# Kernel optimization log

Hardware: AMD Instinct MI355X
Metric: run time of the kernel (lower is better)

The kernel has to match this reference:

```python
import jax, jax.numpy as jnp
import numpy as np

N_NODES = 50000
N_EDGES = 800000
D = 128


def setup_inputs() -> dict:
    key = jax.random.key(0)
    ks = jax.random.split(key, 8)
    scale = 1.0 / np.sqrt(D)
    return {
        "x": jax.random.normal(ks[0], (N_NODES, D), jnp.float32),
        "src": jax.random.randint(ks[1], (N_EDGES,), 0, N_NODES, jnp.int64 if jax.config.jax_enable_x64 else jnp.int32),
        "dst": jax.random.randint(ks[2], (N_EDGES,), 0, N_NODES, jnp.int64 if jax.config.jax_enable_x64 else jnp.int32),
        "W_self0": jax.random.normal(ks[3], (D, D), jnp.float32) * scale,
        "W_neigh0": jax.random.normal(ks[4], (D, D), jnp.float32) * scale,
        "b0": jnp.zeros((D,), jnp.float32),
        "W_self1": jax.random.normal(ks[5], (D, D), jnp.float32) * scale,
        "W_neigh1": jax.random.normal(ks[6], (D, D), jnp.float32) * scale,
        "b1": jnp.zeros((D,), jnp.float32),
    }


def _sage_conv(h, src, dst, W_self, W_neigh, b, n_nodes):
    # mean aggregation over incoming edges (DGL copy_u + mean; isolated nodes -> 0)
    msg = h[src]                                             # [E, d]
    agg = jax.ops.segment_sum(msg, dst, num_segments=n_nodes)  # [N, d]
    deg = jax.ops.segment_sum(jnp.ones((src.shape[0],), h.dtype), dst, num_segments=n_nodes)
    h_neigh = agg / jnp.maximum(deg, 1.0)[:, None]
    return h @ W_self + h_neigh @ W_neigh + b


def reference(x, src, dst, W_self0, W_neigh0, b0, W_self1, W_neigh1, b1):
    n = x.shape[0]
    h = jax.nn.relu(_sage_conv(x, src, dst, W_self0, W_neigh0, b0, n))
    h = jax.nn.relu(_sage_conv(h, src, dst, W_self1, W_neigh1, b1, n))
    # torch F.normalize(p=2, dim=1): x / max(||x||_2, eps)
    norm = jnp.sqrt(jnp.sum(h * h, axis=1, keepdims=True))
    return h / jnp.maximum(norm, 1e-12)
```

## Files before the change

### kernel.cpp

```cpp
#include <hip/hip_runtime.h>

#define NN 50000
#define D 128
#define BM 32
#define SL 6250

typedef unsigned int uint;
typedef unsigned short ushort;
typedef __attribute__((ext_vector_type(8))) short bf16x8;
typedef __attribute__((ext_vector_type(4))) float f32x4;

static __device__ __forceinline__ ushort f2bf(float f) {
    uint u = __float_as_uint(f);
    u = (u + 0x7FFFu + ((u >> 16) & 1u)) >> 16;
    return (ushort)u;
}

#define ADD8(a, u)                                                  \
    {                                                               \
        a[0] += __uint_as_float((u).x << 16);                       \
        a[1] += __uint_as_float((u).x & 0xFFFF0000u);               \
        a[2] += __uint_as_float((u).y << 16);                       \
        a[3] += __uint_as_float((u).y & 0xFFFF0000u);               \
        a[4] += __uint_as_float((u).z << 16);                       \
        a[5] += __uint_as_float((u).z & 0xFFFF0000u);               \
        a[6] += __uint_as_float((u).w << 16);                       \
        a[7] += __uint_as_float((u).w & 0xFFFF0000u);               \
    }

static __device__ __forceinline__ int ladr(int r, int ch) {
    return r * D + (((ch) ^ (r & 7)) << 3);
}

__global__ __launch_bounds__(256) void k_prep(
    const float* __restrict__ x, ushort* __restrict__ xb,
    const float* __restrict__ W0, const float* __restrict__ W1,
    const float* __restrict__ W2, const float* __restrict__ W3,
    ushort* __restrict__ P,
    const int* __restrict__ dst, int* __restrict__ hist, int E)
{
    const int bid = blockIdx.x;
    if (bid < 3125) {
        const int t = bid * 256 + threadIdx.x;
        const float4* p = reinterpret_cast<const float4*>(x) + (size_t)t * 2;
        const float4 v0 = p[0], v1 = p[1];
        uint4 u;
        u.x = (uint)f2bf(v0.x) | ((uint)f2bf(v0.y) << 16);
        u.y = (uint)f2bf(v0.z) | ((uint)f2bf(v0.w) << 16);
        u.z = (uint)f2bf(v1.x) | ((uint)f2bf(v1.y) << 16);
        u.w = (uint)f2bf(v1.z) | ((uint)f2bf(v1.w) << 16);
        reinterpret_cast<uint4*>(xb)[t] = u;
    } else if (bid < 3125 + 256) {
        const int o = (bid - 3125) * 256 + threadIdx.x;
        const int mat = o >> 14;
        const int idx = o & 16383;
        const int kt = idx >> 12;
        const int n  = (idx >> 5) & 127;
        const int ks = idx & 31;
        const float* W = (mat == 0) ? W0 : (mat == 1) ? W1 : (mat == 2) ? W2 : W3;
        P[o] = f2bf(W[(kt * 32 + ks) * D + n]);
    } else {
        const int hb = bid - (3125 + 256);
        const int s = hb & 7;
        const int lo = s * SL, hi = lo + SL;
        const int bs = hb >> 3;
        for (int e = bs * 256 + (int)threadIdx.x; e < E; e += 128 * 256) {
            const int d = dst[e];
            if (d >= lo && d < hi) atomicAdd(&hist[d], 1);
        }
    }
}

__global__ __launch_bounds__(256) void k_bsum(const int* __restrict__ hist,
                                              int* __restrict__ bsum, int n) {
    const int t = threadIdx.x;
    const int i0 = blockIdx.x * 512 + t * 2;
    int s = 0;
    if (i0 < n) s += hist[i0];
    if (i0 + 1 < n) s += hist[i0 + 1];
    #pragma unroll
    for (int o = 1; o < 64; o <<= 1) s += __shfl_xor(s, o);
    __shared__ int wsum[4];
    if ((t & 63) == 0) wsum[t >> 6] = s;
    __syncthreads();
    if (t == 0) bsum[blockIdx.x] = wsum[0] + wsum[1] + wsum[2] + wsum[3];
}

__global__ __launch_bounds__(128) void k_bscan(int* __restrict__ bsum, int nb) {
    const int t = threadIdx.x;
    const int lane = t & 63, w = t >> 6;
    int v = (t < nb) ? bsum[t] : 0;
    int inc = v;
    #pragma unroll
    for (int o = 1; o < 64; o <<= 1) { int u = __shfl_up(inc, o); if (lane >= o) inc += u; }
    __shared__ int wsum[2];
    if (lane == 63) wsum[w] = inc;
    __syncthreads();
    int off = (w == 1) ? wsum[0] : 0;
    if (t < nb) bsum[t] = off + inc - v;
}

__global__ __launch_bounds__(256) void k_apply(const int* __restrict__ hist,
        const int* __restrict__ bsum, int* __restrict__ row_off,
        int* __restrict__ cursor, int n, int E) {
    const int t = threadIdx.x;
    const int i0 = blockIdx.x * 512 + t * 2;
    const int v0 = (i0 < n) ? hist[i0] : 0;
    const int v1 = (i0 + 1 < n) ? hist[i0 + 1] : 0;
    const int s = v0 + v1;
    const int lane = t & 63, w = t >> 6;
    int inc = s;
    #pragma unroll
    for (int o = 1; o < 64; o <<= 1) { int u = __shfl_up(inc, o); if (lane >= o) inc += u; }
    __shared__ int wsum[4], woff[4];
    if (lane == 63) wsum[w] = inc;
    __syncthreads();
    if (t == 0) { int r = 0; for (int k = 0; k < 4; ++k) { woff[k] = r; r += wsum[k]; } }
    __syncthreads();
    const int ex = bsum[blockIdx.x] + woff[w] + (inc - s);
    if (i0 < n)     { row_off[i0] = ex;          cursor[i0] = ex; }
    if (i0 + 1 < n) { row_off[i0 + 1] = ex + v0; cursor[i0 + 1] = ex + v0; }
    if (blockIdx.x == 0 && t == 0) row_off[n] = E;
}

__global__ __launch_bounds__(256) void k_fill_s(const int* __restrict__ src,
        const int* __restrict__ dst, int* __restrict__ cursor,
        int* __restrict__ csr, int E) {
    const int s = blockIdx.x & 7;
    const int lo = s * SL, hi = lo + SL;
    const int bs = blockIdx.x >> 3;
    const int stride = (gridDim.x >> 3) * 256;
    for (int e = bs * 256 + (int)threadIdx.x; e < E; e += stride) {
        const int d = dst[e];
        const int sv = src[e];
        if (d >= lo && d < hi) {
            const int p = atomicAdd(&cursor[d], 1);
            csr[p] = sv;
        }
    }
}

template<bool NORM>
__global__ __launch_bounds__(512, 4) void k_sage(
    const ushort* __restrict__ hb,
    const int* __restrict__ csr, const int* __restrict__ row_off,
    const ushort* __restrict__ Wps, const ushort* __restrict__ Wpn,
    const float* __restrict__ bias, ushort* __restrict__ outb,
    float* __restrict__ out, int n, int E)
{
    __shared__ __align__(16) ushort hsb[BM * D];
    __shared__ __align__(16) ushort hnb[BM * D];
    __shared__ float outt[BM * 132];
    const int row0 = blockIdx.x * BM;
    const int tid = threadIdx.x;
    const int l = tid & 63;
    const int w = tid >> 6;

    {
        const int r = tid >> 4;
        const int ch = tid & 15;
        const int g = row0 + r;
        uint4 u = make_uint4(0u, 0u, 0u, 0u);
        if (g < n) u = *reinterpret_cast<const uint4*>(hb + (size_t)g * D + ch * 8);
        *reinterpret_cast<uint4*>(&hsb[ladr(r, ch)]) = u;
    }

    {
        const int r = tid >> 4;
        const int ql = tid & 15;
        const int g = row0 + r;
        int i = 0, e = 0;
        if (g < n) { i = row_off[g]; e = row_off[g + 1]; }
        const float invd = (e > i) ? 1.0f / (float)(e - i) : 0.0f;
        float a[8];
        #pragma unroll
        for (int j = 0; j < 8; ++j) a[j] = 0.f;
        const size_t off = (size_t)(ql * 8);
        for (; i + 3 < e; i += 4) {
            const int s0 = csr[i], s1 = csr[i + 1], s2 = csr[i + 2], s3 = csr[i + 3];
            const uint4 u0 = *reinterpret_cast<const uint4*>(hb + (size_t)s0 * D + off);
            const uint4 u1 = *reinterpret_cast<const uint4*>(hb + (size_t)s1 * D + off);
            const uint4 u2 = *reinterpret_cast<const uint4*>(hb + (size_t)s2 * D + off);
            const uint4 u3 = *reinterpret_cast<const uint4*>(hb + (size_t)s3 * D + off);
            ADD8(a, u0); ADD8(a, u1); ADD8(a, u2); ADD8(a, u3);
        }
        for (; i < e; ++i) {
            const int s0 = csr[i];
            const uint4 u0 = *reinterpret_cast<const uint4*>(hb + (size_t)s0 * D + off);
            ADD8(a, u0);
        }
        uint4 u;
        u.x = (uint)f2bf(a[0] * invd) | ((uint)f2bf(a[1] * invd) << 16);
        u.y = (uint)f2bf(a[2] * invd) | ((uint)f2bf(a[3] * invd) << 16);
        u.z = (uint)f2bf(a[4] * invd) | ((uint)f2bf(a[5] * invd) << 16);
        u.w = (uint)f2bf(a[6] * invd) | ((uint)f2bf(a[7] * invd) << 16);
        *reinterpret_cast<uint4*>(&hnb[ladr(r, ql)]) = u;
    }
    __syncthreads();

    {
        const int mt = w >> 2;
        const int ntA = (w & 3) * 2;
        const int rA = mt * 16 + (l & 15);
        const int kg = l >> 4;
        f32x4 acc0 = {0.f, 0.f, 0.f, 0.f};
        f32x4 acc1 = {0.f, 0.f, 0.f, 0.f};
        #pragma unroll
        for (int kt = 0; kt < 4; ++kt) {
            const int kc = kt * 4 + kg;
            const bf16x8 as = *reinterpret_cast<const bf16x8*>(&hsb[ladr(rA, kc)]);
            const bf16x8 an = *reinterpret_cast<const bf16x8*>(&hnb[ladr(rA, kc)]);
            const size_t wo0 = (size_t)(kt * 128 + ntA * 16 + (l & 15)) * 32 + kg * 8;
            const size_t wo1 = wo0 + 16 * 32;
            const bf16x8 bs0 = *reinterpret_cast<const bf16x8*>(Wps + wo0);
            const bf16x8 bn0 = *reinterpret_cast<const bf16x8*>(Wpn + wo0);
            const bf16x8 bs1 = *reinterpret_cast<const bf16x8*>(Wps + wo1);
            const bf16x8 bn1 = *reinterpret_cast<const bf16x8*>(Wpn + wo1);
            acc0 = __builtin_amdgcn_mfma_f32_16x16x32_bf16(as, bs0, acc0, 0, 0, 0);
            acc0 = __builtin_amdgcn_mfma_f32_16x16x32_bf16(an, bn0, acc0, 0, 0, 0);
            acc1 = __builtin_amdgcn_mfma_f32_16x16x32_bf16(as, bs1, acc1, 0, 0, 0);
            acc1 = __builtin_amdgcn_mfma_f32_16x16x32_bf16(an, bn1, acc1, 0, 0, 0);
        }
        const int c0 = ntA * 16 + (l & 15);
        const float bv0 = bias[c0], bv1 = bias[c0 + 16];
        #pragma unroll
        for (int i2 = 0; i2 < 4; ++i2) {
            const int rr = mt * 16 + kg * 4 + i2;
            outt[rr * 132 + c0]      = fmaxf(acc0[i2] + bv0, 0.f);
            outt[rr * 132 + c0 + 16] = fmaxf(acc1[i2] + bv1, 0.f);
        }
    }
    __syncthreads();

    {
        const int r = tid >> 4;
        const int c = (tid & 15) * 8;
        const int g = row0 + r;
        float4 v0 = *reinterpret_cast<const float4*>(&outt[r * 132 + c]);
        float4 v1 = *reinterpret_cast<const float4*>(&outt[r * 132 + c + 4]);
        if (!NORM) {
            if (g < n) {
                uint4 u;
                u.x = (uint)f2bf(v0.x) | ((uint)f2bf(v0.y) << 16);
                u.y = (uint)f2bf(v0.z) | ((uint)f2bf(v0.w) << 16);
                u.z = (uint)f2bf(v1.x) | ((uint)f2bf(v1.y) << 16);
                u.w = (uint)f2bf(v1.z) | ((uint)f2bf(v1.w) << 16);
                *reinterpret_cast<uint4*>(outb + (size_t)g * D + c) = u;
            }
        } else {
            float ssq = v0.x * v0.x + v0.y * v0.y + v0.z * v0.z + v0.w * v0.w
                      + v1.x * v1.x + v1.y * v1.y + v1.z * v1.z + v1.w * v1.w;
            #pragma unroll
            for (int o = 1; o < 16; o <<= 1) ssq += __shfl_xor(ssq, o);
            const float scale = 1.0f / fmaxf(sqrtf(ssq), 1e-12f);
            if (g < n) {
                v0.x *= scale; v0.y *= scale; v0.z *= scale; v0.w *= scale;
                v1.x *= scale; v1.y *= scale; v1.z *= scale; v1.w *= scale;
                *reinterpret_cast<float4*>(out + (size_t)g * D + c)     = v0;
                *reinterpret_cast<float4*>(out + (size_t)g * D + c + 4) = v1;
            }
        }
    }
}

extern "C" void kernel_launch(void* const* d_in, const int* in_sizes, int n_in,
                              void* d_out, int out_size, void* d_ws, size_t ws_size,
                              hipStream_t stream) {
    const float* x   = (const float*)d_in[0];
    const int*   src = (const int*)d_in[1];
    const int*   dst = (const int*)d_in[2];
    const float* Ws0 = (const float*)d_in[3];
    const float* Wn0 = (const float*)d_in[4];
    const float* b0  = (const float*)d_in[5];
    const float* Ws1 = (const float*)d_in[6];
    const float* Wn1 = (const float*)d_in[7];
    const float* b1  = (const float*)d_in[8];
    float* out = (float*)d_out;
    const int E = in_sizes[1];

    ushort* xb     = (ushort*)d_ws;
    ushort* h1b    = xb + (size_t)NN * D;
    ushort* Wp     = h1b + (size_t)NN * D;
    int*    hist   = (int*)(Wp + 65536);
    int*    bsum   = hist + NN;
    int*    row_off= bsum + 128;
    int*    cursor = row_off + NN + 1;
    int*    csr    = cursor + NN;

    ushort* Wps0 = Wp;
    ushort* Wpn0 = Wp + 16384;
    ushort* Wps1 = Wp + 32768;
    ushort* Wpn1 = Wp + 49152;

    const int nb = (NN + 511) / 512;

    hipMemsetAsync(hist, 0, (size_t)NN * sizeof(int), stream);
    k_prep<<<3125 + 256 + 1024, 256, 0, stream>>>(x, xb, Ws0, Wn0, Ws1, Wn1, Wp,
                                                  dst, hist, E);
    k_bsum<<<nb, 256, 0, stream>>>(hist, bsum, NN);
    k_bscan<<<1, 128, 0, stream>>>(bsum, nb);
    k_apply<<<nb, 256, 0, stream>>>(hist, bsum, row_off, cursor, NN, E);
    k_fill_s<<<1024, 256, 0, stream>>>(src, dst, cursor, csr, E);

    k_sage<false><<<(NN + BM - 1) / BM, 512, 0, stream>>>(
        xb, csr, row_off, Wps0, Wpn0, b0, h1b, nullptr, NN, E);

    k_sage<true><<<(NN + BM - 1) / BM, 512, 0, stream>>>(
        h1b, csr, row_off, Wps1, Wpn1, b1, nullptr, out, NN, E);
}
```

Measured before the change: 178.1 us.

## Halve SAGE row tile, split neighbor gather across two lanes, fuse scan kernels

```diff
diff --git a/kernel.cpp b/kernel.cpp
--- a/kernel.cpp
+++ b/kernel.cpp
@@ -2,7 +2,7 @@
 
 #define NN 50000
 #define D 128
-#define BM 32
+#define BM 16
 #define SL 6250
 
 typedef unsigned int uint;
@@ -86,38 +86,34 @@
     if (t == 0) bsum[blockIdx.x] = wsum[0] + wsum[1] + wsum[2] + wsum[3];
 }
 
-__global__ __launch_bounds__(128) void k_bscan(int* __restrict__ bsum, int nb) {
+__global__ __launch_bounds__(256) void k_scanapply(const int* __restrict__ hist,
+        const int* __restrict__ bsum, int* __restrict__ row_off,
+        int* __restrict__ cursor, int n, int E, int nb) {
     const int t = threadIdx.x;
     const int lane = t & 63, w = t >> 6;
-    int v = (t < nb) ? bsum[t] : 0;
-    int inc = v;
+    __shared__ int red[4], wsum[4], woff[4], baseS;
+
+    int v = (t < nb && t < blockIdx.x) ? bsum[t] : 0;
     #pragma unroll
-    for (int o = 1; o < 64; o <<= 1) { int u = __shfl_up(inc, o); if (lane >= o) inc += u; }
-    __shared__ int wsum[2];
-    if (lane == 63) wsum[w] = inc;
-    __syncthreads();
-    int off = (w == 1) ? wsum[0] : 0;
-    if (t < nb) bsum[t] = off + inc - v;
-}
-
-__global__ __launch_bounds__(256) void k_apply(const int* __restrict__ hist,
-        const int* __restrict__ bsum, int* __restrict__ row_off,
-        int* __restrict__ cursor, int n, int E) {
-    const int t = threadIdx.x;
+    for (int o = 1; o < 64; o <<= 1) v += __shfl_xor(v, o);
+    if (lane == 0) red[w] = v;
+    __syncthreads();
+    if (t == 0) baseS = red[0] + red[1] + red[2] + red[3];
+    __syncthreads();
+    const int base = baseS;
+
     const int i0 = blockIdx.x * 512 + t * 2;
     const int v0 = (i0 < n) ? hist[i0] : 0;
     const int v1 = (i0 + 1 < n) ? hist[i0 + 1] : 0;
     const int s = v0 + v1;
-    const int lane = t & 63, w = t >> 6;
     int inc = s;
     #pragma unroll
     for (int o = 1; o < 64; o <<= 1) { int u = __shfl_up(inc, o); if (lane >= o) inc += u; }
-    __shared__ int wsum[4], woff[4];
     if (lane == 63) wsum[w] = inc;
     __syncthreads();
     if (t == 0) { int r = 0; for (int k = 0; k < 4; ++k) { woff[k] = r; r += wsum[k]; } }
     __syncthreads();
-    const int ex = bsum[blockIdx.x] + woff[w] + (inc - s);
+    const int ex = base + woff[w] + (inc - s);
     if (i0 < n)     { row_off[i0] = ex;          cursor[i0] = ex; }
     if (i0 + 1 < n) { row_off[i0 + 1] = ex + v0; cursor[i0 + 1] = ex + v0; }
     if (blockIdx.x == 0 && t == 0) row_off[n] = E;
@@ -156,7 +152,7 @@
     const int l = tid & 63;
     const int w = tid >> 6;
 
-    {
+    if (tid < 256) {
         const int r = tid >> 4;
         const int ch = tid & 15;
         const int g = row0 + r;
@@ -166,73 +162,86 @@
     }
 
     {
-        const int r = tid >> 4;
+        const int r = tid >> 5;
+        const int half = (tid >> 4) & 1;
         const int ql = tid & 15;
         const int g = row0 + r;
-        int i = 0, e = 0;
-        if (g < n) { i = row_off[g]; e = row_off[g + 1]; }
-        const float invd = (e > i) ? 1.0f / (float)(e - i) : 0.0f;
+        const int Em1 = E - 1;
+        int beg = 0, end = 0;
+        if (g < n) { beg = row_off[g]; end = row_off[g + 1]; }
+        const float invd = (end > beg) ? 1.0f / (float)(end - beg) : 0.0f;
         float a[8];
         #pragma unroll
         for (int j = 0; j < 8; ++j) a[j] = 0.f;
         const size_t off = (size_t)(ql * 8);
-        for (; i + 3 < e; i += 4) {
-            const int s0 = csr[i], s1 = csr[i + 1], s2 = csr[i + 2], s3 = csr[i + 3];
-            const uint4 u0 = *reinterpret_cast<const uint4*>(hb + (size_t)s0 * D + off);
-            const uint4 u1 = *reinterpret_cast<const uint4*>(hb + (size_t)s1 * D + off);
-            const uint4 u2 = *reinterpret_cast<const uint4*>(hb + (size_t)s2 * D + off);
-            const uint4 u3 = *reinterpret_cast<const uint4*>(hb + (size_t)s3 * D + off);
-            ADD8(a, u0); ADD8(a, u1); ADD8(a, u2); ADD8(a, u3);
-        }
-        for (; i < e; ++i) {
-            const int s0 = csr[i];
-            const uint4 u0 = *reinterpret_cast<const uint4*>(hb + (size_t)s0 * D + off);
-            ADD8(a, u0);
-        }
-        uint4 u;
-        u.x = (uint)f2bf(a[0] * invd) | ((uint)f2bf(a[1] * invd) << 16);
-        u.y = (uint)f2bf(a[2] * invd) | ((uint)f2bf(a[3] * invd) << 16);
-        u.z = (uint)f2bf(a[4] * invd) | ((uint)f2bf(a[5] * invd) << 16);
-        u.w = (uint)f2bf(a[6] * invd) | ((uint)f2bf(a[7] * invd) << 16);
-        *reinterpret_cast<uint4*>(&hnb[ladr(r, ql)]) = u;
+
+        int i = beg + half * 4;
+        if (i + 3 < end) {
+            int s0 = csr[i], s1 = csr[i + 1], s2 = csr[i + 2], s3 = csr[i + 3];
+            while (true) {
+                const uint4 u0 = *reinterpret_cast<const uint4*>(hb + (size_t)s0 * D + off);
+                const uint4 u1 = *reinterpret_cast<const uint4*>(hb + (size_t)s1 * D + off);
+                const uint4 u2 = *reinterpret_cast<const uint4*>(hb + (size_t)s2 * D + off);
+                const uint4 u3 = *reinterpret_cast<const uint4*>(hb + (size_t)s3 * D + off);
+                i += 8;
+                const bool more = (i + 3 < end);
+                int t0, t1, t2, t3;
+                if (more) {
+                    t0 = csr[i]; t1 = csr[i + 1]; t2 = csr[i + 2]; t3 = csr[i + 3];
+                } else {
+                    t0 = csr[min(i + 0, Em1)]; t1 = csr[min(i + 1, Em1)];
+                    t2 = csr[min(i + 2, Em1)]; t3 = csr[min(i + 3, Em1)];
+                }
+                ADD8(a, u0); ADD8(a, u1); ADD8(a, u2); ADD8(a, u3);
+                if (!more) break;
+                s0 = t0; s1 = t1; s2 = t2; s3 = t3;
+            }
+        }
+        const int te = min(i + 4, end);
+        for (int j = i; j < te; ++j) {
+            const int s = csr[j];
+            const uint4 u = *reinterpret_cast<const uint4*>(hb + (size_t)s * D + off);
+            ADD8(a, u);
+        }
+        #pragma unroll
+        for (int j = 0; j < 8; ++j) a[j] += __shfl_xor(a[j], 16);
+        if (half == 0) {
+            uint4 u;
+            u.x = (uint)f2bf(a[0] * invd) | ((uint)f2bf(a[1] * invd) << 16);
+            u.y = (uint)f2bf(a[2] * invd) | ((uint)f2bf(a[3] * invd) << 16);
+            u.z = (uint)f2bf(a[4] * invd) | ((uint)f2bf(a[5] * invd) << 16);
+            u.w = (uint)f2bf(a[6] * invd) | ((uint)f2bf(a[7] * invd) << 16);
+            *reinterpret_cast<uint4*>(&hnb[ladr(r, ql)]) = u;
+        }
     }
     __syncthreads();
 
     {
-        const int mt = w >> 2;
-        const int ntA = (w & 3) * 2;
-        const int rA = mt * 16 + (l & 15);
+        const int rA = l & 15;
         const int kg = l >> 4;
-        f32x4 acc0 = {0.f, 0.f, 0.f, 0.f};
-        f32x4 acc1 = {0.f, 0.f, 0.f, 0.f};
+        f32x4 acc = {0.f, 0.f, 0.f, 0.f};
         #pragma unroll
         for (int kt = 0; kt < 4; ++kt) {
             const int kc = kt * 4 + kg;
             const bf16x8 as = *reinterpret_cast<const bf16x8*>(&hsb[ladr(rA, kc)]);
             const bf16x8 an = *reinterpret_cast<const bf16x8*>(&hnb[ladr(rA, kc)]);
-            const size_t wo0 = (size_t)(kt * 128 + ntA * 16 + (l & 15)) * 32 + kg * 8;
-            const size_t wo1 = wo0 + 16 * 32;
-            const bf16x8 bs0 = *reinterpret_cast<const bf16x8*>(Wps + wo0);
-            const bf16x8 bn0 = *reinterpret_cast<const bf16x8*>(Wpn + wo0);
-            const bf16x8 bs1 = *reinterpret_cast<const bf16x8*>(Wps + wo1);
-            const bf16x8 bn1 = *reinterpret_cast<const bf16x8*>(Wpn + wo1);
-            acc0 = __builtin_amdgcn_mfma_f32_16x16x32_bf16(as, bs0, acc0, 0, 0, 0);
-            acc0 = __builtin_amdgcn_mfma_f32_16x16x32_bf16(an, bn0, acc0, 0, 0, 0);
-            acc1 = __builtin_amdgcn_mfma_f32_16x16x32_bf16(as, bs1, acc1, 0, 0, 0);
-            acc1 = __builtin_amdgcn_mfma_f32_16x16x32_bf16(an, bn1, acc1, 0, 0, 0);
-        }
-        const int c0 = ntA * 16 + (l & 15);
-        const float bv0 = bias[c0], bv1 = bias[c0 + 16];
+            const size_t wo = (size_t)(kt * 128 + w * 16 + rA) * 32 + kg * 8;
+            const bf16x8 bs = *reinterpret_cast<const bf16x8*>(Wps + wo);
+            const bf16x8 bn = *reinterpret_cast<const bf16x8*>(Wpn + wo);
+            acc = __builtin_amdgcn_mfma_f32_16x16x32_bf16(as, bs, acc, 0, 0, 0);
+            acc = __builtin_amdgcn_mfma_f32_16x16x32_bf16(an, bn, acc, 0, 0, 0);
+        }
+        const int c0 = w * 16 + rA;
+        const float bv = bias[c0];
         #pragma unroll
         for (int i2 = 0; i2 < 4; ++i2) {
-            const int rr = mt * 16 + kg * 4 + i2;
-            outt[rr * 132 + c0]      = fmaxf(acc0[i2] + bv0, 0.f);
-            outt[rr * 132 + c0 + 16] = fmaxf(acc1[i2] + bv1, 0.f);
-        }
-    }
-    __syncthreads();
-
-    {
+            const int rr = kg * 4 + i2;
+            outt[rr * 132 + c0] = fmaxf(acc[i2] + bv, 0.f);
+        }
+    }
+    __syncthreads();
+
+    if (tid < 256) {
         const int r = tid >> 4;
         const int c = (tid & 15) * 8;
         const int g = row0 + r;
@@ -298,8 +307,7 @@
     k_prep<<<3125 + 256 + 1024, 256, 0, stream>>>(x, xb, Ws0, Wn0, Ws1, Wn1, Wp,
                                                   dst, hist, E);
     k_bsum<<<nb, 256, 0, stream>>>(hist, bsum, NN);
-    k_bscan<<<1, 128, 0, stream>>>(bsum, nb);
-    k_apply<<<nb, 256, 0, stream>>>(hist, bsum, row_off, cursor, NN, E);
+    k_scanapply<<<nb, 256, 0, stream>>>(hist, bsum, row_off, cursor, NN, E, nb);
     k_fill_s<<<1024, 256, 0, stream>>>(src, dst, cursor, csr, E);
 
     k_sage<false><<<(NN + BM - 1) / BM, 512, 0, stream>>>(
```

Measured after the change: 183.1 us. +2.8%, slower.

## Split neighbor gather into sliced-layout pull kernel and fuse scan kernels

Applied to the files above, without the earlier changes.

```diff
diff --git a/kernel.cpp b/kernel.cpp
--- a/kernel.cpp
+++ b/kernel.cpp
@@ -32,6 +32,10 @@
     return r * D + (((ch) ^ (r & 7)) << 3);
 }
 
+static __device__ __forceinline__ size_t badr(int g, int ch) {
+    return ((size_t)(ch >> 1) * NN + g) * 16 + (ch & 1) * 8;
+}
+
 __global__ __launch_bounds__(256) void k_prep(
     const float* __restrict__ x, ushort* __restrict__ xb,
     const float* __restrict__ W0, const float* __restrict__ W1,
@@ -42,6 +46,8 @@
     const int bid = blockIdx.x;
     if (bid < 3125) {
         const int t = bid * 256 + threadIdx.x;
+        const int node = t >> 4;
+        const int ch = t & 15;
         const float4* p = reinterpret_cast<const float4*>(x) + (size_t)t * 2;
         const float4 v0 = p[0], v1 = p[1];
         uint4 u;
@@ -49,7 +55,7 @@
         u.y = (uint)f2bf(v0.z) | ((uint)f2bf(v0.w) << 16);
         u.z = (uint)f2bf(v1.x) | ((uint)f2bf(v1.y) << 16);
         u.w = (uint)f2bf(v1.z) | ((uint)f2bf(v1.w) << 16);
-        reinterpret_cast<uint4*>(xb)[t] = u;
+        *reinterpret_cast<uint4*>(xb + badr(node, ch)) = u;
     } else if (bid < 3125 + 256) {
         const int o = (bid - 3125) * 256 + threadIdx.x;
         const int mat = o >> 14;
@@ -86,38 +92,34 @@
     if (t == 0) bsum[blockIdx.x] = wsum[0] + wsum[1] + wsum[2] + wsum[3];
 }
 
-__global__ __launch_bounds__(128) void k_bscan(int* __restrict__ bsum, int nb) {
+__global__ __launch_bounds__(256) void k_scanapply(const int* __restrict__ hist,
+        const int* __restrict__ bsum, int* __restrict__ row_off,
+        int* __restrict__ cursor, int n, int E, int nb) {
     const int t = threadIdx.x;
     const int lane = t & 63, w = t >> 6;
-    int v = (t < nb) ? bsum[t] : 0;
-    int inc = v;
+    __shared__ int red[4], wsum[4], woff[4], baseS;
+
+    int v = (t < nb && t < blockIdx.x) ? bsum[t] : 0;
     #pragma unroll
-    for (int o = 1; o < 64; o <<= 1) { int u = __shfl_up(inc, o); if (lane >= o) inc += u; }
-    __shared__ int wsum[2];
-    if (lane == 63) wsum[w] = inc;
-    __syncthreads();
-    int off = (w == 1) ? wsum[0] : 0;
-    if (t < nb) bsum[t] = off + inc - v;
-}
-
-__global__ __launch_bounds__(256) void k_apply(const int* __restrict__ hist,
-        const int* __restrict__ bsum, int* __restrict__ row_off,
-        int* __restrict__ cursor, int n, int E) {
-    const int t = threadIdx.x;
+    for (int o = 1; o < 64; o <<= 1) v += __shfl_xor(v, o);
+    if (lane == 0) red[w] = v;
+    __syncthreads();
+    if (t == 0) baseS = red[0] + red[1] + red[2] + red[3];
+    __syncthreads();
+    const int base = baseS;
+
     const int i0 = blockIdx.x * 512 + t * 2;
     const int v0 = (i0 < n) ? hist[i0] : 0;
     const int v1 = (i0 + 1 < n) ? hist[i0 + 1] : 0;
     const int s = v0 + v1;
-    const int lane = t & 63, w = t >> 6;
     int inc = s;
     #pragma unroll
     for (int o = 1; o < 64; o <<= 1) { int u = __shfl_up(inc, o); if (lane >= o) inc += u; }
-    __shared__ int wsum[4], woff[4];
     if (lane == 63) wsum[w] = inc;
     __syncthreads();
     if (t == 0) { int r = 0; for (int k = 0; k < 4; ++k) { woff[k] = r; r += wsum[k]; } }
     __syncthreads();
-    const int ex = bsum[blockIdx.x] + woff[w] + (inc - s);
+    const int ex = base + woff[w] + (inc - s);
     if (i0 < n)     { row_off[i0] = ex;          cursor[i0] = ex; }
     if (i0 + 1 < n) { row_off[i0 + 1] = ex + v0; cursor[i0 + 1] = ex + v0; }
     if (blockIdx.x == 0 && t == 0) row_off[n] = E;
@@ -140,13 +142,52 @@
     }
 }
 
+__global__ __launch_bounds__(256) void k_pull_s(
+    const ushort* __restrict__ hbS, const int* __restrict__ csr,
+    const int* __restrict__ row_off, ushort* __restrict__ aggS, int E)
+{
+    const int s = blockIdx.x & 7;
+    const int blk = blockIdx.x >> 3;
+    const int rg0 = blk * 128 + ((int)threadIdx.x >> 1);
+    const int c = threadIdx.x & 1;
+    const int co = c * 8;
+    const ushort* base = hbS + (size_t)s * NN * 16;
+    ushort* abase = aggS + (size_t)s * NN * 16;
+
+    for (int g = rg0; g < NN; g += 16384) {
+        int i = row_off[g];
+        const int e = row_off[g + 1];
+        const float invd = (e > i) ? 1.0f / (float)(e - i) : 0.0f;
+        float a[8];
+        #pragma unroll
+        for (int j = 0; j < 8; ++j) a[j] = 0.f;
+        for (; i + 3 < e; i += 4) {
+            const int s0 = csr[i], s1 = csr[i + 1], s2 = csr[i + 2], s3 = csr[i + 3];
+            const uint4 u0 = *reinterpret_cast<const uint4*>(base + (size_t)s0 * 16 + co);
+            const uint4 u1 = *reinterpret_cast<const uint4*>(base + (size_t)s1 * 16 + co);
+            const uint4 u2 = *reinterpret_cast<const uint4*>(base + (size_t)s2 * 16 + co);
+            const uint4 u3 = *reinterpret_cast<const uint4*>(base + (size_t)s3 * 16 + co);
+            ADD8(a, u0); ADD8(a, u1); ADD8(a, u2); ADD8(a, u3);
+        }
+        for (; i < e; ++i) {
+            const uint4 u = *reinterpret_cast<const uint4*>(base + (size_t)csr[i] * 16 + co);
+            ADD8(a, u);
+        }
+        uint4 u;
+        u.x = (uint)f2bf(a[0] * invd) | ((uint)f2bf(a[1] * invd) << 16);
+        u.y = (uint)f2bf(a[2] * invd) | ((uint)f2bf(a[3] * invd) << 16);
+        u.z = (uint)f2bf(a[4] * invd) | ((uint)f2bf(a[5] * invd) << 16);
+        u.w = (uint)f2bf(a[6] * invd) | ((uint)f2bf(a[7] * invd) << 16);
+        *reinterpret_cast<uint4*>(abase + (size_t)g * 16 + co) = u;
+    }
+}
+
 template<bool NORM>
 __global__ __launch_bounds__(512, 4) void k_sage(
-    const ushort* __restrict__ hb,
-    const int* __restrict__ csr, const int* __restrict__ row_off,
+    const ushort* __restrict__ hbS, const ushort* __restrict__ aggS,
     const ushort* __restrict__ Wps, const ushort* __restrict__ Wpn,
-    const float* __restrict__ bias, ushort* __restrict__ outb,
-    float* __restrict__ out, int n, int E)
+    const float* __restrict__ bias, ushort* __restrict__ outbS,
+    float* __restrict__ out, int n)
 {
     __shared__ __align__(16) ushort hsb[BM * D];
     __shared__ __align__(16) ushort hnb[BM * D];
@@ -160,41 +201,15 @@
         const int r = tid >> 4;
         const int ch = tid & 15;
         const int g = row0 + r;
-        uint4 u = make_uint4(0u, 0u, 0u, 0u);
-        if (g < n) u = *reinterpret_cast<const uint4*>(hb + (size_t)g * D + ch * 8);
-        *reinterpret_cast<uint4*>(&hsb[ladr(r, ch)]) = u;
-    }
-
-    {
-        const int r = tid >> 4;
-        const int ql = tid & 15;
-        const int g = row0 + r;
-        int i = 0, e = 0;
-        if (g < n) { i = row_off[g]; e = row_off[g + 1]; }
-        const float invd = (e > i) ? 1.0f / (float)(e - i) : 0.0f;
-        float a[8];
-        #pragma unroll
-        for (int j = 0; j < 8; ++j) a[j] = 0.f;
-        const size_t off = (size_t)(ql * 8);
-        for (; i + 3 < e; i += 4) {
-            const int s0 = csr[i], s1 = csr[i + 1], s2 = csr[i + 2], s3 = csr[i + 3];
-            const uint4 u0 = *reinterpret_cast<const uint4*>(hb + (size_t)s0 * D + off);
-            const uint4 u1 = *reinterpret_cast<const uint4*>(hb + (size_t)s1 * D + off);
-            const uint4 u2 = *reinterpret_cast<const uint4*>(hb + (size_t)s2 * D + off);
-            const uint4 u3 = *reinterpret_cast<const uint4*>(hb + (size_t)s3 * D + off);
-            ADD8(a, u0); ADD8(a, u1); ADD8(a, u2); ADD8(a, u3);
-        }
-        for (; i < e; ++i) {
-            const int s0 = csr[i];
-            const uint4 u0 = *reinterpret_cast<const uint4*>(hb + (size_t)s0 * D + off);
-            ADD8(a, u0);
-        }
-        uint4 u;
-        u.x = (uint)f2bf(a[0] * invd) | ((uint)f2bf(a[1] * invd) << 16);
-        u.y = (uint)f2bf(a[2] * invd) | ((uint)f2bf(a[3] * invd) << 16);
-        u.z = (uint)f2bf(a[4] * invd) | ((uint)f2bf(a[5] * invd) << 16);
-        u.w = (uint)f2bf(a[6] * invd) | ((uint)f2bf(a[7] * invd) << 16);
-        *reinterpret_cast<uint4*>(&hnb[ladr(r, ql)]) = u;
+        uint4 us = make_uint4(0u, 0u, 0u, 0u);
+        uint4 un = make_uint4(0u, 0u, 0u, 0u);
+        if (g < n) {
+            const size_t o = badr(g, ch);
+            us = *reinterpret_cast<const uint4*>(hbS + o);
+            un = *reinterpret_cast<const uint4*>(aggS + o);
+        }
+        *reinterpret_cast<uint4*>(&hsb[ladr(r, ch)]) = us;
+        *reinterpret_cast<uint4*>(&hnb[ladr(r, ch)]) = un;
     }
     __syncthreads();
 
@@ -234,7 +249,8 @@
 
     {
         const int r = tid >> 4;
-        const int c = (tid & 15) * 8;
+        const int ch = tid & 15;
+        const int c = ch * 8;
         const int g = row0 + r;
         float4 v0 = *reinterpret_cast<const float4*>(&outt[r * 132 + c]);
         float4 v1 = *reinterpret_cast<const float4*>(&outt[r * 132 + c + 4]);
@@ -245,7 +261,7 @@
                 u.y = (uint)f2bf(v0.z) | ((uint)f2bf(v0.w) << 16);
                 u.z = (uint)f2bf(v1.x) | ((uint)f2bf(v1.y) << 16);
                 u.w = (uint)f2bf(v1.z) | ((uint)f2bf(v1.w) << 16);
-                *reinterpret_cast<uint4*>(outb + (size_t)g * D + c) = u;
+                *reinterpret_cast<uint4*>(outbS + badr(g, ch)) = u;
             }
         } else {
             float ssq = v0.x * v0.x + v0.y * v0.y + v0.z * v0.z + v0.w * v0.w
@@ -287,6 +303,9 @@
     int*    cursor = row_off + NN + 1;
     int*    csr    = cursor + NN;
 
+    ushort* agg1 = (ushort*)d_out;
+    ushort* agg2 = xb;
+
     ushort* Wps0 = Wp;
     ushort* Wpn0 = Wp + 16384;
     ushort* Wps1 = Wp + 32768;
@@ -298,13 +317,14 @@
     k_prep<<<3125 + 256 + 1024, 256, 0, stream>>>(x, xb, Ws0, Wn0, Ws1, Wn1, Wp,
                                                   dst, hist, E);
     k_bsum<<<nb, 256, 0, stream>>>(hist, bsum, NN);
-    k_bscan<<<1, 128, 0, stream>>>(bsum, nb);
-    k_apply<<<nb, 256, 0, stream>>>(hist, bsum, row_off, cursor, NN, E);
+    k_scanapply<<<nb, 256, 0, stream>>>(hist, bsum, row_off, cursor, NN, E, nb);
     k_fill_s<<<1024, 256, 0, stream>>>(src, dst, cursor, csr, E);
 
+    k_pull_s<<<1024, 256, 0, stream>>>(xb, csr, row_off, agg1, E);
     k_sage<false><<<(NN + BM - 1) / BM, 512, 0, stream>>>(
-        xb, csr, row_off, Wps0, Wpn0, b0, h1b, nullptr, NN, E);
-
+        xb, agg1, Wps0, Wpn0, b0, h1b, nullptr, NN);
+
+    k_pull_s<<<1024, 256, 0, stream>>>(h1b, csr, row_off, agg2, E);
     k_sage<true><<<(NN + BM - 1) / BM, 512, 0, stream>>>(
-        h1b, csr, row_off, Wps1, Wpn1, b1, nullptr, out, NN, E);
-}
+        h1b, agg2, Wps1, Wpn1, b1, nullptr, out, NN);
+}
```

Result: slower. 211.6 us (+18.8%).

## Fuse block scan into apply kernel, move conversions there, unroll gather by 8

Applied to the files above, without the earlier changes.

```diff
diff --git a/kernel.cpp b/kernel.cpp
--- a/kernel.cpp
+++ b/kernel.cpp
@@ -32,42 +32,14 @@
     return r * D + (((ch) ^ (r & 7)) << 3);
 }
 
-__global__ __launch_bounds__(256) void k_prep(
-    const float* __restrict__ x, ushort* __restrict__ xb,
-    const float* __restrict__ W0, const float* __restrict__ W1,
-    const float* __restrict__ W2, const float* __restrict__ W3,
-    ushort* __restrict__ P,
-    const int* __restrict__ dst, int* __restrict__ hist, int E)
-{
-    const int bid = blockIdx.x;
-    if (bid < 3125) {
-        const int t = bid * 256 + threadIdx.x;
-        const float4* p = reinterpret_cast<const float4*>(x) + (size_t)t * 2;
-        const float4 v0 = p[0], v1 = p[1];
-        uint4 u;
-        u.x = (uint)f2bf(v0.x) | ((uint)f2bf(v0.y) << 16);
-        u.y = (uint)f2bf(v0.z) | ((uint)f2bf(v0.w) << 16);
-        u.z = (uint)f2bf(v1.x) | ((uint)f2bf(v1.y) << 16);
-        u.w = (uint)f2bf(v1.z) | ((uint)f2bf(v1.w) << 16);
-        reinterpret_cast<uint4*>(xb)[t] = u;
-    } else if (bid < 3125 + 256) {
-        const int o = (bid - 3125) * 256 + threadIdx.x;
-        const int mat = o >> 14;
-        const int idx = o & 16383;
-        const int kt = idx >> 12;
-        const int n  = (idx >> 5) & 127;
-        const int ks = idx & 31;
-        const float* W = (mat == 0) ? W0 : (mat == 1) ? W1 : (mat == 2) ? W2 : W3;
-        P[o] = f2bf(W[(kt * 32 + ks) * D + n]);
-    } else {
-        const int hb = bid - (3125 + 256);
-        const int s = hb & 7;
-        const int lo = s * SL, hi = lo + SL;
-        const int bs = hb >> 3;
-        for (int e = bs * 256 + (int)threadIdx.x; e < E; e += 128 * 256) {
-            const int d = dst[e];
-            if (d >= lo && d < hi) atomicAdd(&hist[d], 1);
-        }
+__global__ __launch_bounds__(256) void k_hist_s(const int* __restrict__ dst,
+                                                int* __restrict__ hist, int E) {
+    const int s = blockIdx.x & 7;
+    const int lo = s * SL, hi = lo + SL;
+    const int bs = blockIdx.x >> 3;
+    for (int e = bs * 256 + (int)threadIdx.x; e < E; e += 128 * 256) {
+        const int d = dst[e];
+        if (d >= lo && d < hi) atomicAdd(&hist[d], 1);
     }
 }
 
@@ -86,41 +58,65 @@
     if (t == 0) bsum[blockIdx.x] = wsum[0] + wsum[1] + wsum[2] + wsum[3];
 }
 
-__global__ __launch_bounds__(128) void k_bscan(int* __restrict__ bsum, int nb) {
+__global__ __launch_bounds__(256) void k_scanapply_f(
+    const int* __restrict__ hist, const int* __restrict__ bsum,
+    int* __restrict__ row_off, int* __restrict__ cursor, int n, int E, int nb,
+    const float* __restrict__ x, ushort* __restrict__ xb,
+    const float* __restrict__ W0, const float* __restrict__ W1,
+    const float* __restrict__ W2, const float* __restrict__ W3,
+    ushort* __restrict__ P)
+{
+    const int bid = blockIdx.x;
     const int t = threadIdx.x;
-    const int lane = t & 63, w = t >> 6;
-    int v = (t < nb) ? bsum[t] : 0;
-    int inc = v;
-    #pragma unroll
-    for (int o = 1; o < 64; o <<= 1) { int u = __shfl_up(inc, o); if (lane >= o) inc += u; }
-    __shared__ int wsum[2];
-    if (lane == 63) wsum[w] = inc;
-    __syncthreads();
-    int off = (w == 1) ? wsum[0] : 0;
-    if (t < nb) bsum[t] = off + inc - v;
-}
-
-__global__ __launch_bounds__(256) void k_apply(const int* __restrict__ hist,
-        const int* __restrict__ bsum, int* __restrict__ row_off,
-        int* __restrict__ cursor, int n, int E) {
-    const int t = threadIdx.x;
-    const int i0 = blockIdx.x * 512 + t * 2;
-    const int v0 = (i0 < n) ? hist[i0] : 0;
-    const int v1 = (i0 + 1 < n) ? hist[i0 + 1] : 0;
-    const int s = v0 + v1;
-    const int lane = t & 63, w = t >> 6;
-    int inc = s;
-    #pragma unroll
-    for (int o = 1; o < 64; o <<= 1) { int u = __shfl_up(inc, o); if (lane >= o) inc += u; }
-    __shared__ int wsum[4], woff[4];
-    if (lane == 63) wsum[w] = inc;
-    __syncthreads();
-    if (t == 0) { int r = 0; for (int k = 0; k < 4; ++k) { woff[k] = r; r += wsum[k]; } }
-    __syncthreads();
-    const int ex = bsum[blockIdx.x] + woff[w] + (inc - s);
-    if (i0 < n)     { row_off[i0] = ex;          cursor[i0] = ex; }
-    if (i0 + 1 < n) { row_off[i0 + 1] = ex + v0; cursor[i0 + 1] = ex + v0; }
-    if (blockIdx.x == 0 && t == 0) row_off[n] = E;
+    if (bid < nb) {
+        const int sb = bid;
+        const int lane = t & 63, w = t >> 6;
+        __shared__ int red[4], wsum[4], woff[4], baseS;
+
+        int v = (t < nb && t < sb) ? bsum[t] : 0;
+        #pragma unroll
+        for (int o = 1; o < 64; o <<= 1) v += __shfl_xor(v, o);
+        if (lane == 0) red[w] = v;
+        __syncthreads();
+        if (t == 0) baseS = red[0] + red[1] + red[2] + red[3];
+        __syncthreads();
+        const int base = baseS;
+
+        const int i0 = sb * 512 + t * 2;
+        const int v0 = (i0 < n) ? hist[i0] : 0;
+        const int v1 = (i0 + 1 < n) ? hist[i0 + 1] : 0;
+        const int s = v0 + v1;
+        int inc = s;
+        #pragma unroll
+        for (int o = 1; o < 64; o <<= 1) { int u = __shfl_up(inc, o); if (lane >= o) inc += u; }
+        if (lane == 63) wsum[w] = inc;
+        __syncthreads();
+        if (t == 0) { int r = 0; for (int k = 0; k < 4; ++k) { woff[k] = r; r += wsum[k]; } }
+        __syncthreads();
+        const int ex = base + woff[w] + (inc - s);
+        if (i0 < n)     { row_off[i0] = ex;          cursor[i0] = ex; }
+        if (i0 + 1 < n) { row_off[i0 + 1] = ex + v0; cursor[i0 + 1] = ex + v0; }
+        if (sb == 0 && t == 0) row_off[n] = E;
+    } else if (bid < nb + 3125) {
+        const int tt = (bid - nb) * 256 + t;
+        const float4* p = reinterpret_cast<const float4*>(x) + (size_t)tt * 2;
+        const float4 v0 = p[0], v1 = p[1];
+        uint4 u;
+        u.x = (uint)f2bf(v0.x) | ((uint)f2bf(v0.y) << 16);
+        u.y = (uint)f2bf(v0.z) | ((uint)f2bf(v0.w) << 16);
+        u.z = (uint)f2bf(v1.x) | ((uint)f2bf(v1.y) << 16);
+        u.w = (uint)f2bf(v1.z) | ((uint)f2bf(v1.w) << 16);
+        reinterpret_cast<uint4*>(xb)[tt] = u;
+    } else {
+        const int o = (bid - nb - 3125) * 256 + t;
+        const int mat = o >> 14;
+        const int idx = o & 16383;
+        const int kt = idx >> 12;
+        const int nn = (idx >> 5) & 127;
+        const int ks = idx & 31;
+        const float* W = (mat == 0) ? W0 : (mat == 1) ? W1 : (mat == 2) ? W2 : W3;
+        P[o] = f2bf(W[(kt * 32 + ks) * D + nn]);
+    }
 }
 
 __global__ __launch_bounds__(256) void k_fill_s(const int* __restrict__ src,
@@ -176,6 +172,20 @@
         #pragma unroll
         for (int j = 0; j < 8; ++j) a[j] = 0.f;
         const size_t off = (size_t)(ql * 8);
+        for (; i + 7 < e; i += 8) {
+            const int s0 = csr[i],     s1 = csr[i + 1], s2 = csr[i + 2], s3 = csr[i + 3];
+            const int s4 = csr[i + 4], s5 = csr[i + 5], s6 = csr[i + 6], s7 = csr[i + 7];
+            const uint4 u0 = *reinterpret_cast<const uint4*>(hb + (size_t)s0 * D + off);
+            const uint4 u1 = *reinterpret_cast<const uint4*>(hb + (size_t)s1 * D + off);
+            const uint4 u2 = *reinterpret_cast<const uint4*>(hb + (size_t)s2 * D + off);
+            const uint4 u3 = *reinterpret_cast<const uint4*>(hb + (size_t)s3 * D + off);
+            const uint4 u4 = *reinterpret_cast<const uint4*>(hb + (size_t)s4 * D + off);
+            const uint4 u5 = *reinterpret_cast<const uint4*>(hb + (size_t)s5 * D + off);
+            const uint4 u6 = *reinterpret_cast<const uint4*>(hb + (size_t)s6 * D + off);
+            const uint4 u7 = *reinterpret_cast<const uint4*>(hb + (size_t)s7 * D + off);
+            ADD8(a, u0); ADD8(a, u1); ADD8(a, u2); ADD8(a, u3);
+            ADD8(a, u4); ADD8(a, u5); ADD8(a, u6); ADD8(a, u7);
+        }
         for (; i + 3 < e; i += 4) {
             const int s0 = csr[i], s1 = csr[i + 1], s2 = csr[i + 2], s3 = csr[i + 3];
             const uint4 u0 = *reinterpret_cast<const uint4*>(hb + (size_t)s0 * D + off);
@@ -295,11 +305,11 @@
     const int nb = (NN + 511) / 512;
 
     hipMemsetAsync(hist, 0, (size_t)NN * sizeof(int), stream);
-    k_prep<<<3125 + 256 + 1024, 256, 0, stream>>>(x, xb, Ws0, Wn0, Ws1, Wn1, Wp,
-                                                  dst, hist, E);
+    k_hist_s<<<1024, 256, 0, stream>>>(dst, hist, E);
     k_bsum<<<nb, 256, 0, stream>>>(hist, bsum, NN);
-    k_bscan<<<1, 128, 0, stream>>>(bsum, nb);
-    k_apply<<<nb, 256, 0, stream>>>(hist, bsum, row_off, cursor, NN, E);
+    k_scanapply_f<<<nb + 3125 + 256, 256, 0, stream>>>(
+        hist, bsum, row_off, cursor, NN, E, nb,
+        x, xb, Ws0, Wn0, Ws1, Wn1, Wp);
     k_fill_s<<<1024, 256, 0, stream>>>(src, dst, cursor, csr, E);
 
     k_sage<false><<<(NN + BM - 1) / BM, 512, 0, stream>>>(
```

Result: slower. 189.8 us (+6.6%).
